# Performance work log

Hardware: AMD Instinct MI355X
Metric: run time of the kernel (lower is better)

The kernel has to match this reference:

```python
import jax, jax.numpy as jnp
import numpy as np

S, G, N, E = 4, 3, 20000, 320000   # seq_len, num_graphs, nodes, edges
DIN = HID = OUT = 64


def setup_inputs() -> dict:
    key = jax.random.key(0)
    ks = jax.random.split(key, 12)
    s = 0.1  # weight scale ~ Glorot-ish for d=64
    return {
        "x": jax.random.normal(ks[0], (S, G, N, DIN), jnp.float32),
        "edge_index": jax.random.randint(ks[1], (S, G, 2, E), 0, N, dtype=jnp.int32),
        "W1l": jax.random.normal(ks[2], (G, DIN, HID), jnp.float32) * s,
        "W1r": jax.random.normal(ks[3], (G, DIN, HID), jnp.float32) * s,
        "b1": jnp.zeros((G, HID), jnp.float32),
        "W2l": jax.random.normal(ks[4], (G, HID, OUT), jnp.float32) * s,
        "W2r": jax.random.normal(ks[5], (G, HID, OUT), jnp.float32) * s,
        "b2": jnp.zeros((G, OUT), jnp.float32),
        "Wih": jax.random.normal(ks[6], (4 * OUT, OUT), jnp.float32) * s,
        "Whh": jax.random.normal(ks[7], (4 * OUT, OUT), jnp.float32) * s,
        "bih": jnp.zeros((4 * OUT,), jnp.float32),
        "bhh": jnp.zeros((4 * OUT,), jnp.float32),
    }


def _sage(x, ei, Wl, Wr, b):
    # PyG SAGEConv(aggr='mean'): out = mean_{j->i}(x_j) @ Wl + x_i @ Wr + b
    src, dst = ei[0], ei[1]
    n = x.shape[0]
    msg = jax.ops.segment_sum(x[src], dst, num_segments=n)          # [N, d]
    cnt = jax.ops.segment_sum(jnp.ones((ei.shape[1], 1), x.dtype), dst, num_segments=n)
    mean = jnp.where(cnt > 0, msg / jnp.maximum(cnt, 1.0), 0.0)
    return mean @ Wl + x @ Wr + b


def _gnn(x, ei, Wl1, Wr1, bb1, Wl2, Wr2, bb2):
    h = jnp.tanh(_sage(x, ei, Wl1, Wr1, bb1))
    return jnp.tanh(_sage(h, ei, Wl2, Wr2, bb2))


def reference(x, edge_index, W1l, W1r, b1, W2l, W2r, b2, Wih, Whh, bih, bhh):
    # vmap over graphs (each graph has its own conv weights), then over timesteps
    per_graph = jax.vmap(_gnn, in_axes=(0, 0, 0, 0, 0, 0, 0, 0))
    per_seq = jax.vmap(per_graph, in_axes=(0, 0, None, None, None, None, None, None))
    h = per_seq(x, edge_index, W1l, W1r, b1, W2l, W2r, b2)          # [S, G, N, OUT]
    # torch: per timestep stack graphs [G,N,O] -> transpose -> [N,G,O]; cat over seq on dim0
    lstm_in = jnp.transpose(h, (0, 2, 1, 3)).reshape(S * N, G, OUT)  # [B, T=G, OUT]
    B = lstm_in.shape[0]

    def step(carry, xt):
        hp, cp = carry
        gates = xt @ Wih.T + hp @ Whh.T + bih + bhh                 # [B, 4*OUT]
        i, f, g, o = jnp.split(gates, 4, axis=-1)                   # torch gate order i,f,g,o
        c = jax.nn.sigmoid(f) * cp + jax.nn.sigmoid(i) * jnp.tanh(g)
        hn = jax.nn.sigmoid(o) * jnp.tanh(c)
        return (hn, c), None

    init = (jnp.zeros((B, OUT), x.dtype), jnp.zeros((B, OUT), x.dtype))
    (h_last, _), _ = jax.lax.scan(step, init, jnp.transpose(lstm_in, (1, 0, 2)))
    return h_last  # [S*N, OUT] == lstm_out[:, -1, :].squeeze()
```

## Files before the change

### kernel.cpp

```cpp
#include <hip/hip_runtime.h>
#include <math.h>

#define S 4
#define G 3
#define NN 20000
#define EE 320000
#define D 64
#define SG (S*G)

#define RGS 32
#define RNODES2 625
#define BCAP 14336
#define CHUNKA 100

#define LTILES 313
#define LTASKS (12*LTILES)
#define LQ (LTASKS/8)
#define LR (LTASKS%8)
#define NGRP   (NN/16)

static __device__ __forceinline__ float rcpf(float x){ return __builtin_amdgcn_rcpf(x); }
static __device__ __forceinline__ float sigmf(float x){ return rcpf(1.0f + __expf(-x)); }
static __device__ __forceinline__ float tanhf_fast(float x){
    float t = __expf(2.0f*x);
    return 1.0f - 2.0f*rcpf(t + 1.0f);
}

static __device__ __forceinline__ unsigned short f2bf(float f){
    union { float f; unsigned u; } v; v.f = f;
    unsigned r = v.u + 0x7FFF + ((v.u >> 16) & 1);
    return (unsigned short)(r >> 16);
}

typedef short bf16x8 __attribute__((ext_vector_type(8)));
typedef float f32x4  __attribute__((ext_vector_type(4)));


__global__ __launch_bounds__(256) void binA_kernel(const int* __restrict__ ei,
                                                   int* __restrict__ bcur,
                                                   int* __restrict__ bkt){
    __shared__ int wcnt[4*RGS];
    __shared__ int wb[4*RGS];
    int chunk = blockIdx.x, sg = blockIdx.y;
    int tid = threadIdx.x, w = tid >> 6;
    const int* srcp = ei + (size_t)(sg*2 + 0)*EE;
    const int* dstp = ei + (size_t)(sg*2 + 1)*EE;
    const int EPC = EE/CHUNKA;
    int start = chunk*EPC, end = start + EPC;

    for (int it = 0; it < (EPC + 1023)/1024; ++it){
        if (tid < 4*RGS) wcnt[tid] = 0;
        __syncthreads();
        int e = start + it*1024 + tid*4;
        bool valid = e < end;
        int d_[4], s_[4], r_[4], dl_[4], rk_[4];
        if (valid){
            int4 d4 = *(const int4*)&dstp[e];
            int4 s4 = *(const int4*)&srcp[e];
            d_[0]=d4.x; d_[1]=d4.y; d_[2]=d4.z; d_[3]=d4.w;
            s_[0]=s4.x; s_[1]=s4.y; s_[2]=s4.z; s_[3]=s4.w;
            #pragma unroll
            for (int j = 0; j < 4; ++j){
                int r = d_[j] / RNODES2;
                r_[j]  = r;
                dl_[j] = d_[j] - r*RNODES2;
                rk_[j] = atomicAdd(&wcnt[w*RGS + r], 1);
            }
        }
        __syncthreads();
        if (tid < RGS){
            int c0 = wcnt[0*RGS+tid], c1 = wcnt[1*RGS+tid];
            int c2 = wcnt[2*RGS+tid], c3 = wcnt[3*RGS+tid];
            int tot = c0+c1+c2+c3;
            int gb = 0;
            if (tot > 0) gb = atomicAdd(&bcur[sg*RGS + tid], tot);
            wb[0*RGS+tid] = gb;
            wb[1*RGS+tid] = gb + c0;
            wb[2*RGS+tid] = gb + c0 + c1;
            wb[3*RGS+tid] = gb + c0 + c1 + c2;
        }
        __syncthreads();
        if (valid){
            #pragma unroll
            for (int j = 0; j < 4; ++j){
                int pos = wb[w*RGS + r_[j]] + rk_[j];
                if (pos < BCAP)
                    bkt[(size_t)(sg*RGS + r_[j])*BCAP + pos] = (dl_[j] << 15) | s_[j];
            }
        }
    }
}


__global__ __launch_bounds__(256) void buildB_kernel(int* __restrict__ bkt,
                                                     const int* __restrict__ bcur,
                                                     int* __restrict__ off2,
                                                     int* __restrict__ deg2,
                                                     int* __restrict__ nid2,
                                                     int* __restrict__ offU){
    __shared__ int hist[RNODES2];
    __shared__ int pref[RNODES2];
    __shared__ int seg[BCAP];
    __shared__ int sums[256];
    __shared__ int dh[64];
    int sg = blockIdx.x / RGS, rg = blockIdx.x % RGS;
    int tid = threadIdx.x;
    int cnt = bcur[sg*RGS + rg];
    if (cnt > BCAP) cnt = BCAP;
    size_t base = (size_t)(sg*RGS + rg)*BCAP;
    int gnode = sg*NN + rg*RNODES2;

    for (int i = tid; i < RNODES2; i += 256) hist[i] = 0;
    if (tid < 64) dh[tid] = 0;
    __syncthreads();
    for (int j = tid; j < cnt; j += 256)
        atomicAdd(&hist[bkt[base + j] >> 15], 1);
    __syncthreads();

    int lo = tid*3, hi = min(lo+3, RNODES2);
    int s = 0;
    for (int i = lo; i < hi; ++i) s += (hist[i] + 3) & ~3;
    sums[tid] = s; __syncthreads();
    for (int ofs = 1; ofs < 256; ofs <<= 1){
        int v = (tid >= ofs) ? sums[tid-ofs] : 0;
        __syncthreads();
        sums[tid] += v;
        __syncthreads();
    }
    int run = sums[tid] - s;
    for (int i = lo; i < hi; ++i){
        pref[i] = run;
        offU[gnode + i] = (int)base + run;
        run += (hist[i] + 3) & ~3;
    }
    __syncthreads();

    for (int i = tid; i < RNODES2; i += 256)
        atomicAdd(&dh[min(hist[i], 63)], 1);
    __syncthreads();
    if (tid == 0){
        int r = 0;
        for (int k = 0; k < 64; ++k){ int c = dh[k]; dh[k] = r; r += c; }
    }
    __syncthreads();
    for (int i = tid; i < RNODES2; i += 256){
        int pos = atomicAdd(&dh[min(hist[i], 63)], 1);
        off2[gnode + pos] = offU[gnode + i];
        deg2[gnode + pos] = hist[i];
        nid2[gnode + pos] = rg*RNODES2 + i;
    }
    __syncthreads();

    for (int j = tid; j < cnt; j += 256){
        int p = bkt[base + j];
        int slot = atomicAdd(&pref[p >> 15], 1);
        if (slot < BCAP) seg[slot] = p & 0x7FFF;
    }
    __syncthreads();

    int padtot = min(sums[255], BCAP);
    for (int j = tid; j < padtot; j += 256) bkt[base + j] = seg[j];
}


__global__ __launch_bounds__(256) void convert_kernel(const float* __restrict__ x,
                                                      unsigned short* __restrict__ xb){
    int idx = blockIdx.x*256 + threadIdx.x;
    if (idx >= SG*NN*16) return;
    float4 v = ((const float4*)x)[idx];
    uint2 pk;
    pk.x = (unsigned)f2bf(v.x) | ((unsigned)f2bf(v.y) << 16);
    pk.y = (unsigned)f2bf(v.z) | ((unsigned)f2bf(v.w) << 16);
    ((uint2*)xb)[idx] = pk;
}


__global__ __launch_bounds__(256) void wprep2_kernel(const float* __restrict__ W1l,
                                                     const float* __restrict__ W1r,
                                                     const float* __restrict__ W2l,
                                                     const float* __restrict__ W2r,
                                                     const float* __restrict__ Wih,
                                                     const float* __restrict__ Whh,
                                                     const float* __restrict__ bih,
                                                     const float* __restrict__ bhh,
                                                     unsigned short* __restrict__ WL1,
                                                     unsigned short* __restrict__ WL2,
                                                     unsigned short* __restrict__ Wt,
                                                     float* __restrict__ bc){
    int idx = blockIdx.x*256 + threadIdx.x;
    if (idx < 24576){
        int g = idx >> 13, rem = idx & 8191, col = rem >> 7, k = rem & 127;
        float v = (k < 64) ? W1l[((size_t)g*64 + k)*64 + col]
                           : W1r[((size_t)g*64 + (k-64))*64 + col];
        WL1[idx] = f2bf(v);
    } else if (idx < 49152){
        int t = idx - 24576;
        int g = t >> 13, rem = t & 8191, col = rem >> 7, k = rem & 127;
        float v = (k < 64) ? W2l[((size_t)g*64 + k)*64 + col]
                           : W2r[((size_t)g*64 + (k-64))*64 + col];
        WL2[t] = f2bf(v);
    } else if (idx < 81920){
        int t = idx - 49152;
        int col = t >> 7, k = t & 127;
        float v = (k < 64) ? Wih[col*64 + k] : Whh[col*64 + (k - 64)];
        Wt[t] = f2bf(v);
    } else if (idx < 82176){
        int t = idx - 81920;
        bc[t] = bih[t] + bhh[t];
    }
}


#define WP 72

#define LOADC(F, BASE) { \
    int s0_ = (BASE) + (q >> 1); \
    int s1_ = s0_ + 2; \
    int n0_ = csr[a + s0_]; \
    int n1_ = csr[a + s1_]; \
    unsigned o0_ = (s0_ < dg) ? (((unsigned)n0_) << 7) : zoff0; \
    unsigned o1_ = (s1_ < dg) ? (((unsigned)n1_) << 7) : zoff0; \
    o0_ += qh; o1_ += qh; \
    F[0] = *(const bf16x8*)(inbc + o0_); \
    F[1] = *(const bf16x8*)(inbc + o0_ + 32); \
    F[2] = *(const bf16x8*)(inbc + o0_ + 64); \
    F[3] = *(const bf16x8*)(inbc + o0_ + 96); \
    F[4] = *(const bf16x8*)(inbc + o1_); \
    F[5] = *(const bf16x8*)(inbc + o1_ + 32); \
    F[6] = *(const bf16x8*)(inbc + o1_ + 64); \
    F[7] = *(const bf16x8*)(inbc + o1_ + 96); \
}

#define MFMA8(F) { \
    acc[0] = __builtin_amdgcn_mfma_f32_16x16x32_bf16(F[0], BI, acc[0], 0, 0, 0); \
    acc[1] = __builtin_amdgcn_mfma_f32_16x16x32_bf16(F[1], BI, acc[1], 0, 0, 0); \
    acc[2] = __builtin_amdgcn_mfma_f32_16x16x32_bf16(F[2], BI, acc[2], 0, 0, 0); \
    acc[3] = __builtin_amdgcn_mfma_f32_16x16x32_bf16(F[3], BI, acc[3], 0, 0, 0); \
    acc[0] = __builtin_amdgcn_mfma_f32_16x16x32_bf16(F[4], BI, acc[0], 0, 0, 0); \
    acc[1] = __builtin_amdgcn_mfma_f32_16x16x32_bf16(F[5], BI, acc[1], 0, 0, 0); \
    acc[2] = __builtin_amdgcn_mfma_f32_16x16x32_bf16(F[6], BI, acc[2], 0, 0, 0); \
    acc[3] = __builtin_amdgcn_mfma_f32_16x16x32_bf16(F[7], BI, acc[3], 0, 0, 0); \
}

__global__ __launch_bounds__(256,4) void layer_kernel(const unsigned short* __restrict__ xb,
                                                    const int* __restrict__ off2,
                                                    const int* __restrict__ deg2,
                                                    const int* __restrict__ nid2,
                                                    const int* __restrict__ csr,
                                                    const unsigned short* __restrict__ WL,
                                                    const float* __restrict__ bias,
                                                    unsigned short* __restrict__ outb){
    __shared__ unsigned short sM[4][16*WP];
    __shared__ unsigned short sO[4][16*WP];
    int L = blockIdx.x;
    int xcd = L & 7;
    int task = ((xcd < LR) ? xcd*(LQ+1) : LR*(LQ+1) + (xcd-LR)*LQ) + (L >> 3);
    int sg = task / LTILES;
    int tsel = task - sg*LTILES;
    int tile = (LTILES-1) - tsel;
    int g = sg % G;
    int tid = threadIdx.x;
    int wave = tid >> 6, lane = tid & 63;
    int r = lane & 15, q = lane >> 4;
    unsigned qh = (unsigned)((q & 1) << 4);
    const char* inbc = (const char*)(xb + (size_t)sg*NN*D);

    int gid = tile*4 + wave;
    bool wv = (gid < NGRP);

    union { uint4 u; bf16x8 v; } biu;
    {
        unsigned v_ = 0x3F80u << ((r & 1) * 16);
        bool on = ((r >> 3) == (q & 1));
        int w_ = (r & 7) >> 1;
        biu.u.x = (on && w_ == 0) ? v_ : 0u;
        biu.u.y = (on && w_ == 1) ? v_ : 0u;
        biu.u.z = (on && w_ == 2) ? v_ : 0u;
        biu.u.w = (on && w_ == 3) ? v_ : 0u;
    }
    bf16x8 BI = biu.v;

    int idx = sg*NN + gid*16 + r;
    int node = 0, dg = 0, a = 0;
    if (wv){
        node = nid2[idx];
        a    = off2[idx];
        dg   = deg2[idx];
    }
    int mx = dg;
    mx = max(mx, __shfl_xor(mx, 1));
    mx = max(mx, __shfl_xor(mx, 2));
    mx = max(mx, __shfl_xor(mx, 4));
    mx = max(mx, __shfl_xor(mx, 8));

    unsigned zoff0 = (((unsigned)((SG - sg)*NN)) << 7);

    f32x4 acc[4];
    #pragma unroll
    for (int cb = 0; cb < 4; ++cb) acc[cb] = (f32x4){0.f,0.f,0.f,0.f};

    if (mx > 0){
        int nch = (mx + 3) >> 2;
        bf16x8 Fa[8], Fb[8];
        LOADC(Fa, 0);
        for (int c = 0; c < nch; c += 2){
            if (c + 1 < nch) LOADC(Fb, (c + 1)*4);
            MFMA8(Fa);
            if (c + 1 < nch){
                if (c + 2 < nch) LOADC(Fa, (c + 2)*4);
                MFMA8(Fb);
            }
        }
    }

    float inv[4];
    #pragma unroll
    for (int reg = 0; reg < 4; ++reg){
        int d = __shfl(dg, (q << 2) | reg, 16);
        inv[reg] = (d > 0) ? rcpf((float)d) : 0.0f;
    }
    #pragma unroll
    for (int cb = 0; cb < 4; ++cb)
        #pragma unroll
        for (int reg = 0; reg < 4; ++reg)
            sM[wave][(q*4 + reg)*WP + cb*16 + r] = f2bf(acc[cb][reg] * inv[reg]);

    const unsigned short* WLg = WL + (size_t)g*64*128;
    f32x4 accv[4];
    #pragma unroll
    for (int ct = 0; ct < 4; ++ct) accv[ct] = (f32x4){0.f,0.f,0.f,0.f};
    #pragma unroll
    for (int kc = 0; kc < 4; ++kc){
        bf16x8 af;
        if (kc < 2) af = *(const bf16x8*)&sM[wave][r*WP + kc*32 + q*8];
        else        af = *(const bf16x8*)(inbc + (((unsigned)node) << 7) + (unsigned)((kc-2)*64 + q*16));
        #pragma unroll
        for (int ct = 0; ct < 4; ++ct){
            bf16x8 bfr = *(const bf16x8*)&WLg[(ct*16 + r)*128 + kc*32 + q*8];
            accv[ct] = __builtin_amdgcn_mfma_f32_16x16x32_bf16(af, bfr, accv[ct], 0, 0, 0);
        }
    }

    #pragma unroll
    for (int ct = 0; ct < 4; ++ct){
        float bv = bias[g*64 + ct*16 + r];
        #pragma unroll
        for (int reg = 0; reg < 4; ++reg)
            sO[wave][(q*4+reg)*WP + ct*16 + r] = f2bf(tanhf_fast(accv[ct][reg] + bv));
    }
    if (wv){
        #pragma unroll
        for (int pass = 0; pass < 2; ++pass){
            int rloc = pass*8 + (lane >> 3), chunk = lane & 7;
            int i2 = gid*16 + rloc;
            int nd = nid2[sg*NN + i2];
            uint4 v = *(const uint4*)&sO[wave][rloc*WP + chunk*8];
            *(uint4*)&outb[((size_t)sg*NN + nd)*D + chunk*8] = v;
        }
    }
}


__global__ __launch_bounds__(256) void lstm_kernel(const unsigned short* __restrict__ h2b,
                                                   const unsigned short* __restrict__ Wt,
                                                   const float* __restrict__ bc,
                                                   float* __restrict__ out){
    __shared__ unsigned short sH[64*WP];
    int tid = threadIdx.x;
    int b0 = blockIdx.x * 64;
    int wave = tid >> 6, lane = tid & 63;
    int n0 = lane & 15, q = lane >> 4;
    int jcol = wave*16 + n0;

    float bb[4];
    #pragma unroll
    for (int T = 0; T < 4; ++T) bb[T] = bc[T*64 + jcol];

    float c[4][4];
    #pragma unroll
    for (int rt = 0; rt < 4; ++rt)
        #pragma unroll
        for (int reg = 0; reg < 4; ++reg) c[rt][reg] = 0.0f;

    int s_[4], n_[4];
    #pragma unroll
    for (int rt = 0; rt < 4; ++rt){
        int b = b0 + rt*16 + n0;
        s_[rt] = b / NN; n_[rt] = b - s_[rt]*NN;
    }

    #pragma unroll
    for (int t = 0; t < G; ++t){
        f32x4 accv[4][4];
        #pragma unroll
        for (int rt = 0; rt < 4; ++rt)
            #pragma unroll
            for (int T = 0; T < 4; ++T) accv[rt][T] = (f32x4){0.f,0.f,0.f,0.f};

        int nkc = (t == 0) ? 2 : 4;
        #pragma unroll
        for (int kc = 0; kc < 4; ++kc){
            if (kc >= nkc) break;
            bf16x8 af[4];
            #pragma unroll
            for (int rt = 0; rt < 4; ++rt){
                if (kc < 2) af[rt] = *(const bf16x8*)&h2b[((size_t)(s_[rt]*G + t)*NN + n_[rt])*D + kc*32 + q*8];
                else        af[rt] = *(const bf16x8*)&sH[(rt*16 + n0)*WP + (kc-2)*32 + q*8];
            }
            #pragma unroll
            for (int T = 0; T < 4; ++T){
                int ct = T*4 + wave;
                bf16x8 bfr = *(const bf16x8*)&Wt[(ct*16 + n0)*128 + kc*32 + q*8];
                #pragma unroll
                for (int rt = 0; rt < 4; ++rt)
                    accv[rt][T] = __builtin_amdgcn_mfma_f32_16x16x32_bf16(af[rt], bfr, accv[rt][T], 0, 0, 0);
            }
        }
        if (t > 0) __syncthreads();

        #pragma unroll
        for (int rt = 0; rt < 4; ++rt){
            #pragma unroll
            for (int reg = 0; reg < 4; ++reg){
                float ig = sigmf(accv[rt][0][reg] + bb[0]);
                float fg = sigmf(accv[rt][1][reg] + bb[1]);
                float gg = tanhf_fast(accv[rt][2][reg] + bb[2]);
                float og = sigmf(accv[rt][3][reg] + bb[3]);
                float cn = fg*c[rt][reg] + ig*gg;
                c[rt][reg] = cn;
                float hv = og * tanhf_fast(cn);
                int row = rt*16 + q*4 + reg;
                if (t < G-1) sH[row*WP + jcol] = f2bf(hv);
                else         out[(size_t)(b0 + row)*D + jcol] = hv;
            }
        }
        if (t < G-1) __syncthreads();
    }
}


extern "C" void kernel_launch(void* const* d_in, const int* in_sizes, int n_in,
                              void* d_out, int out_size, void* d_ws, size_t ws_size,
                              hipStream_t stream) {
    const float* x   = (const float*)d_in[0];
    const int*   ei  = (const int*)  d_in[1];
    const float* W1l = (const float*)d_in[2];
    const float* W1r = (const float*)d_in[3];
    const float* b1  = (const float*)d_in[4];
    const float* W2l = (const float*)d_in[5];
    const float* W2r = (const float*)d_in[6];
    const float* b2  = (const float*)d_in[7];
    const float* Wih = (const float*)d_in[8];
    const float* Whh = (const float*)d_in[9];
    const float* bih = (const float*)d_in[10];
    const float* bhh = (const float*)d_in[11];
    float* out = (float*)d_out;

    char* ws = (char*)d_ws;
    size_t cur = 0;
    auto alloc = [&](size_t bytes)->void*{
        cur = (cur + 255) & ~(size_t)255;
        void* p = ws + cur; cur += bytes; return p;
    };
    int*   bkt  = (int*)alloc((size_t)SG*RGS*BCAP*4);
    int*   bcur = (int*)alloc((size_t)SG*RGS*4);
    int*   off2 = (int*)alloc((size_t)SG*NN*4);
    int*   deg2 = (int*)alloc((size_t)SG*NN*4);
    int*   nid2 = (int*)alloc((size_t)SG*NN*4);
    int*   offU = (int*)alloc((size_t)SG*NN*4);
    unsigned short* xb  = (unsigned short*)alloc(((size_t)SG*NN + 1)*D*2);
    unsigned short* h1b = (unsigned short*)alloc(((size_t)SG*NN + 1)*D*2);
    unsigned short* h2b = (unsigned short*)alloc((size_t)SG*NN*D*2);
    unsigned short* WL1 = (unsigned short*)alloc((size_t)G*64*128*2);
    unsigned short* WL2 = (unsigned short*)alloc((size_t)G*64*128*2);
    unsigned short* Wt  = (unsigned short*)alloc((size_t)256*128*2);
    float* bc   = (float*)alloc((size_t)256*4);
    (void)ws_size; (void)in_sizes; (void)n_in; (void)out_size;

    (void)hipMemsetAsync(bcur, 0, (size_t)SG*RGS*4, stream);
    (void)hipMemsetAsync(xb  + (size_t)SG*NN*D, 0, (size_t)D*2, stream);
    (void)hipMemsetAsync(h1b + (size_t)SG*NN*D, 0, (size_t)D*2, stream);

    convert_kernel<<<(SG*NN*16 + 255)/256, 256, 0, stream>>>(x, xb);
    binA_kernel  <<<dim3(CHUNKA, SG), 256, 0, stream>>>(ei, bcur, bkt);
    buildB_kernel<<<SG*RGS, 256, 0, stream>>>(bkt, bcur, off2, deg2, nid2, offU);
    wprep2_kernel<<<321, 256, 0, stream>>>(W1l, W1r, W2l, W2r, Wih, Whh, bih, bhh,
                                           WL1, WL2, Wt, bc);

    layer_kernel<<<LTASKS, 256, 0, stream>>>(xb,  off2, deg2, nid2, bkt, WL1, b1, h1b);
    layer_kernel<<<LTASKS, 256, 0, stream>>>(h1b, off2, deg2, nid2, bkt, WL2, b2, h2b);

    lstm_kernel <<<(S*NN)/64, 256, 0, stream>>>(h2b, Wt, bc, out);
}
```

Before: 450.6 us.

## Stage neighbor gathers through swizzled LDS with full-row coalesced loads

Neighbor feature aggregation in the layer kernel now has each lane load 16-byte pieces so that 8 lanes cover a whole 128-byte neighbor row. Rows are written into a per-wave XOR-swizzled LDS staging buffer, then read back in MFMA fragment layout. The old path had each lane pull scattered 16-byte pieces straight from global memory into registers. The change aims for fully coalesced row reads and fewer outstanding scattered loads, but it adds an LDS round trip per chunk and drops the register double-buffering between load and MFMA. LDS use also grows to 32KB per block, which may limit occupancy.

```diff
diff --git a/kernel.cpp b/kernel.cpp
--- a/kernel.cpp
+++ b/kernel.cpp
@@ -212,35 +212,7 @@
 
 
 #define WP 72
-
-#define LOADC(F, BASE) { \
-    int s0_ = (BASE) + (q >> 1); \
-    int s1_ = s0_ + 2; \
-    int n0_ = csr[a + s0_]; \
-    int n1_ = csr[a + s1_]; \
-    unsigned o0_ = (s0_ < dg) ? (((unsigned)n0_) << 7) : zoff0; \
-    unsigned o1_ = (s1_ < dg) ? (((unsigned)n1_) << 7) : zoff0; \
-    o0_ += qh; o1_ += qh; \
-    F[0] = *(const bf16x8*)(inbc + o0_); \
-    F[1] = *(const bf16x8*)(inbc + o0_ + 32); \
-    F[2] = *(const bf16x8*)(inbc + o0_ + 64); \
-    F[3] = *(const bf16x8*)(inbc + o0_ + 96); \
-    F[4] = *(const bf16x8*)(inbc + o1_); \
-    F[5] = *(const bf16x8*)(inbc + o1_ + 32); \
-    F[6] = *(const bf16x8*)(inbc + o1_ + 64); \
-    F[7] = *(const bf16x8*)(inbc + o1_ + 96); \
-}
-
-#define MFMA8(F) { \
-    acc[0] = __builtin_amdgcn_mfma_f32_16x16x32_bf16(F[0], BI, acc[0], 0, 0, 0); \
-    acc[1] = __builtin_amdgcn_mfma_f32_16x16x32_bf16(F[1], BI, acc[1], 0, 0, 0); \
-    acc[2] = __builtin_amdgcn_mfma_f32_16x16x32_bf16(F[2], BI, acc[2], 0, 0, 0); \
-    acc[3] = __builtin_amdgcn_mfma_f32_16x16x32_bf16(F[3], BI, acc[3], 0, 0, 0); \
-    acc[0] = __builtin_amdgcn_mfma_f32_16x16x32_bf16(F[4], BI, acc[0], 0, 0, 0); \
-    acc[1] = __builtin_amdgcn_mfma_f32_16x16x32_bf16(F[5], BI, acc[1], 0, 0, 0); \
-    acc[2] = __builtin_amdgcn_mfma_f32_16x16x32_bf16(F[6], BI, acc[2], 0, 0, 0); \
-    acc[3] = __builtin_amdgcn_mfma_f32_16x16x32_bf16(F[7], BI, acc[3], 0, 0, 0); \
-}
+#define SWZ(e) ((((e) >> 1) ^ ((e) >> 4)) & 7)
 
 __global__ __launch_bounds__(256,4) void layer_kernel(const unsigned short* __restrict__ xb,
                                                     const int* __restrict__ off2,
@@ -250,8 +222,7 @@
                                                     const unsigned short* __restrict__ WL,
                                                     const float* __restrict__ bias,
                                                     unsigned short* __restrict__ outb){
-    __shared__ unsigned short sM[4][16*WP];
-    __shared__ unsigned short sO[4][16*WP];
+    __shared__ unsigned short sStage[4][4096];
     int L = blockIdx.x;
     int xcd = L & 7;
     int task = ((xcd < LR) ? xcd*(LQ+1) : LR*(LQ+1) + (xcd-LR)*LQ) + (L >> 3);
@@ -262,8 +233,8 @@
     int tid = threadIdx.x;
     int wave = tid >> 6, lane = tid & 63;
     int r = lane & 15, q = lane >> 4;
-    unsigned qh = (unsigned)((q & 1) << 4);
     const char* inbc = (const char*)(xb + (size_t)sg*NN*D);
+    unsigned short* stg = &sStage[wave][0];
 
     int gid = tile*4 + wave;
     bool wv = (gid < NGRP);
@@ -295,24 +266,46 @@
 
     unsigned zoff0 = (((unsigned)((SG - sg)*NN)) << 7);
 
+    int aG  = __shfl(a,  lane >> 2);
+    int dgG = __shfl(dg, lane >> 2);
+
     f32x4 acc[4];
     #pragma unroll
     for (int cb = 0; cb < 4; ++cb) acc[cb] = (f32x4){0.f,0.f,0.f,0.f};
 
-    if (mx > 0){
-        int nch = (mx + 3) >> 2;
-        bf16x8 Fa[8], Fb[8];
-        LOADC(Fa, 0);
-        for (int c = 0; c < nch; c += 2){
-            if (c + 1 < nch) LOADC(Fb, (c + 1)*4);
-            MFMA8(Fa);
-            if (c + 1 < nch){
-                if (c + 2 < nch) LOADC(Fa, (c + 2)*4);
-                MFMA8(Fb);
-            }
-        }
-    }
-
+    int nch = (mx + 3) >> 2;
+    for (int c = 0; c < nch; ++c){
+        int sL = c*4 + (lane & 3);
+        int nL = csr[aG + sL];
+        unsigned adr = (sL < dgG) ? (((unsigned)nL) << 7) : zoff0;
+        uint4 v[8];
+        #pragma unroll
+        for (int j = 0; j < 8; ++j){
+            unsigned ae = (unsigned)__shfl((int)adr, j*8 + (lane >> 3));
+            v[j] = *(const uint4*)(inbc + ae + (unsigned)((lane & 7) << 4));
+        }
+        #pragma unroll
+        for (int j = 0; j < 8; ++j){
+            int e = j*8 + (lane >> 3);
+            int gr = ((lane & 7) ^ SWZ(e)) << 4;
+            *(uint4*)((char*)stg + e*128 + gr) = v[j];
+        }
+        #pragma unroll
+        for (int m = 0; m < 2; ++m){
+            int e = r*4 + m*2 + (q >> 1);
+            int ebase = e*128;
+            int sw = SWZ(e) << 4;
+            #pragma unroll
+            for (int cb = 0; cb < 4; ++cb){
+                int b = cb*32 + ((q & 1) << 4);
+                bf16x8 af = *(const bf16x8*)((const char*)stg + ebase + (b ^ sw));
+                acc[cb] = __builtin_amdgcn_mfma_f32_16x16x32_bf16(af, BI, acc[cb], 0, 0, 0);
+            }
+        }
+    }
+
+    asm volatile("" ::: "memory");
+    unsigned short* sMw = stg;
     float inv[4];
     #pragma unroll
     for (int reg = 0; reg < 4; ++reg){
@@ -323,7 +316,8 @@
     for (int cb = 0; cb < 4; ++cb)
         #pragma unroll
         for (int reg = 0; reg < 4; ++reg)
-            sM[wave][(q*4 + reg)*WP + cb*16 + r] = f2bf(acc[cb][reg] * inv[reg]);
+            sMw[(q*4 + reg)*WP + cb*16 + r] = f2bf(acc[cb][reg] * inv[reg]);
+    asm volatile("" ::: "memory");
 
     const unsigned short* WLg = WL + (size_t)g*64*128;
     f32x4 accv[4];
@@ -332,7 +326,7 @@
     #pragma unroll
     for (int kc = 0; kc < 4; ++kc){
         bf16x8 af;
-        if (kc < 2) af = *(const bf16x8*)&sM[wave][r*WP + kc*32 + q*8];
+        if (kc < 2) af = *(const bf16x8*)&sMw[r*WP + kc*32 + q*8];
         else        af = *(const bf16x8*)(inbc + (((unsigned)node) << 7) + (unsigned)((kc-2)*64 + q*16));
         #pragma unroll
         for (int ct = 0; ct < 4; ++ct){
@@ -341,20 +335,23 @@
         }
     }
 
+    asm volatile("" ::: "memory");
+    unsigned short* sOw = stg + 2048;
     #pragma unroll
     for (int ct = 0; ct < 4; ++ct){
         float bv = bias[g*64 + ct*16 + r];
         #pragma unroll
         for (int reg = 0; reg < 4; ++reg)
-            sO[wave][(q*4+reg)*WP + ct*16 + r] = f2bf(tanhf_fast(accv[ct][reg] + bv));
-    }
+            sOw[(q*4+reg)*WP + ct*16 + r] = f2bf(tanhf_fast(accv[ct][reg] + bv));
+    }
+    asm volatile("" ::: "memory");
     if (wv){
         #pragma unroll
         for (int pass = 0; pass < 2; ++pass){
             int rloc = pass*8 + (lane >> 3), chunk = lane & 7;
             int i2 = gid*16 + rloc;
             int nd = nid2[sg*NN + i2];
-            uint4 v = *(const uint4*)&sO[wave][rloc*WP + chunk*8];
+            uint4 v = *(const uint4*)&sOw[rloc*WP + chunk*8];
             *(uint4*)&outb[((size_t)sg*NN + nd)*D + chunk*8] = v;
         }
     }
```

Measured after the change: 382.3 us. 15.2% less time.
